# Optimization experiments

Measured on AMD Instinct MI355X. Metric: run time of the kernel, lower is better.

## Reference

```python
import jax, jax.numpy as jnp
import numpy as np
import math

NUM_EMBED = 1024
EMBED_DIM = 256
COMMITMENT_COST = 0.25


def setup_inputs() -> dict:
    key = jax.random.key(0)
    k1, k2 = jax.random.split(key)
    inputs = jax.random.normal(k1, (16, EMBED_DIM, 4096), dtype=jnp.float32)
    embed = jax.random.normal(k2, (NUM_EMBED, EMBED_DIM), dtype=jnp.float32)
    return {"inputs": inputs, "embed": embed}


def reference(inputs, embed):
    sg = jax.lax.stop_gradient
    num_embed = embed.shape[0]
    # channels-first (B, D, T) -> (B, T, D)
    x = jnp.swapaxes(inputs, 1, -1)
    B, T, D = x.shape
    flat = x.reshape(-1, D)  # (N, D)
    # pairwise squared distances to the codebook: (N, K)
    d2 = (jnp.sum(flat * flat, axis=1, keepdims=True)
          + jnp.sum(embed * embed, axis=1)
          - 2.0 * flat @ embed.T)
    q_idx = jnp.argmin(d2, axis=1)  # (N,) int
    # one-hot @ embed is just a gather of the nearest codewords
    z_q = embed[q_idx].reshape(x.shape)  # (B, T, D)
    vq_loss = jnp.mean((z_q - sg(x)) ** 2)
    commitment_loss = jnp.mean((sg(z_q) - x) ** 2)
    loss = vq_loss + COMMITMENT_COST * commitment_loss
    # straight-through estimator
    z_q_st = x + sg(z_q - x)
    # codebook usage stats: probs = mean of the one-hot rows
    n = flat.shape[0]
    probs = jnp.zeros((num_embed,), dtype=flat.dtype).at[q_idx].add(1.0) / n
    perplexity = jnp.exp(-jnp.sum(probs * jnp.log(probs + 1e-10)))
    num_spatial_positions = n / B  # == T
    kldiv_r = (math.log(num_embed) * num_spatial_positions
               * jnp.ones((B, 1), dtype=x.dtype))
    z_q_out = jnp.swapaxes(z_q_st, 1, -1)  # back to (B, D, T)
    return z_q_out, loss, kldiv_r, perplexity
```

## Files before the change

kernel.cpp:

```cpp
#include <hip/hip_runtime.h>
#include <math.h>

#define T_DIM 4096
#define D_DIM 256
#define K_NUM 1024
#define B_NUM 16
#define N_TOT (B_NUM * T_DIM)
#define EPS_FLAG 0.03f

typedef short short8 __attribute__((ext_vector_type(8)));
typedef float f32x4 __attribute__((ext_vector_type(4)));

#define WS_FLAGCNT 0
#define WS_LOSS 4
#define WS_HIST 64
#define WS_E2 4352
#define WS_QIDX 8704
#define WS_FLAGLIST 270848
#define WS_ESWZ 540672

__device__ inline unsigned short bf16r(float v) {
    unsigned u = __float_as_uint(v);
    unsigned r = u + 0x7FFFu + ((u >> 16) & 1u);
    return (unsigned short)(r >> 16);
}

__device__ inline void gl_lds16(const void* g, void* l) {
    __builtin_amdgcn_global_load_lds(
        (const __attribute__((address_space(1))) unsigned int*)g,
        (__attribute__((address_space(3))) unsigned int*)l, 16, 0, 0);
}

__global__ __launch_bounds__(256) void e2_kernel(const float* __restrict__ embed,
                                                 float* __restrict__ e2) {
    const int wave = threadIdx.x >> 6;
    const int lane = threadIdx.x & 63;
    const int k = blockIdx.x * 4 + wave;
    const float4* row = (const float4*)(embed + (size_t)k * D_DIM);
    float4 v = row[lane];
    float s = v.x * v.x + v.y * v.y + v.z * v.z + v.w * v.w;
    #pragma unroll
    for (int off = 32; off; off >>= 1) s += __shfl_down(s, off);
    if (lane == 0) e2[k] = s;
}

__global__ __launch_bounds__(256) void prep_eswz_kernel(const float* __restrict__ embed,
                                                        unsigned char* __restrict__ eswz) {
    const int tau = blockIdx.x * 256 + threadIdx.x;
    const int g = tau >> 9;
    const int k = (tau >> 6) & 7;
    const int l = tau & 63;
    const int col = g * 16 + (l & 15);
    const int d0 = k * 32 + ((l >> 4) << 3);
    const float* src = embed + (size_t)col * D_DIM + d0;
    short8 hi, lo;
    #pragma unroll
    for (int j = 0; j < 8; ++j) {
        float v = src[j];
        unsigned short hs = bf16r(v);
        float hif = __uint_as_float((unsigned)hs << 16);
        unsigned short ls = bf16r(v - hif);
        hi[j] = (short)hs; lo[j] = (short)ls;
    }
    *(short8*)(eswz + (size_t)g * 16384 + k * 1024 + l * 16) = hi;
    *(short8*)(eswz + (size_t)g * 16384 + 8192 + k * 1024 + l * 16) = lo;
}

__global__ __launch_bounds__(256, 2) void argmin_mfma_kernel(
    const float* __restrict__ x, const unsigned char* __restrict__ eswz,
    const float* __restrict__ e2, int* __restrict__ qidx,
    int* __restrict__ flagcnt, int* __restrict__ flaglist)
{
    __shared__ __align__(16) unsigned char bbuf[2][32768];
    __shared__ float e2s[K_NUM];

    const int tid = threadIdx.x;
    const int w = tid >> 6;
    const int l = tid & 63;
    const int rb = blockIdx.x * 128;
    const int b = rb >> 12;
    const float* xb = x + (size_t)b * (D_DIM * T_DIM);

    {
        const unsigned char* src = eswz + (size_t)tid * 16;
        #pragma unroll
        for (int r = 0; r < 8; ++r) gl_lds16(src + r * 4096, &bbuf[0][tid * 16 + r * 4096]);
    }
    for (int i = tid; i < K_NUM; i += 256) e2s[i] = e2[i];

    short8 Ah[2][8], Al[2][8];
    #pragma unroll
    for (int f = 0; f < 2; ++f) {
        const int row = rb + w * 32 + f * 16 + (l & 15);
        const int t = row & (T_DIM - 1);
        const float* xp = xb + t;
        #pragma unroll
        for (int k = 0; k < 8; ++k) {
            const int d0 = k * 32 + ((l >> 4) << 3);
            short8 hi, lo;
            #pragma unroll
            for (int j = 0; j < 8; ++j) {
                float v = xp[(size_t)(d0 + j) * T_DIM];
                unsigned short hs = bf16r(v);
                float hif = __uint_as_float((unsigned)hs << 16);
                unsigned short ls = bf16r(v - hif);
                hi[j] = (short)hs; lo[j] = (short)ls;
            }
            Ah[f][k] = hi; Al[f][k] = lo;
        }
    }
    __syncthreads();

    float bestv[8], secv[8];
    int   besti[8];
    #pragma unroll
    for (int s = 0; s < 8; ++s) { bestv[s] = 3.4e38f; secv[s] = 3.4e38f; besti[s] = 0x7FFFFFFF; }

    for (int g = 0; g < 32; ++g) {
        if (g + 1 < 32) {
            const unsigned char* src = eswz + (size_t)(g + 1) * 32768 + (size_t)tid * 16;
            unsigned char* dst = &bbuf[(g + 1) & 1][tid * 16];
            #pragma unroll
            for (int r = 0; r < 8; ++r) gl_lds16(src + r * 4096, dst + r * 4096);
        }
        const unsigned char* bb = bbuf[g & 1];

        f32x4 a00 = {0.f,0.f,0.f,0.f}, a01 = {0.f,0.f,0.f,0.f};
        f32x4 a10 = {0.f,0.f,0.f,0.f}, a11 = {0.f,0.f,0.f,0.f};
        #pragma unroll
        for (int k = 0; k < 8; ++k) {
            short8 bh0 = *(const short8*)(bb + k * 1024 + l * 16);
            short8 bl0 = *(const short8*)(bb + 8192 + k * 1024 + l * 16);
            short8 bh1 = *(const short8*)(bb + 16384 + k * 1024 + l * 16);
            short8 bl1 = *(const short8*)(bb + 16384 + 8192 + k * 1024 + l * 16);
            a00 = __builtin_amdgcn_mfma_f32_16x16x32_bf16(Ah[0][k], bh0, a00, 0, 0, 0);
            a10 = __builtin_amdgcn_mfma_f32_16x16x32_bf16(Ah[1][k], bh0, a10, 0, 0, 0);
            a01 = __builtin_amdgcn_mfma_f32_16x16x32_bf16(Ah[0][k], bh1, a01, 0, 0, 0);
            a11 = __builtin_amdgcn_mfma_f32_16x16x32_bf16(Ah[1][k], bh1, a11, 0, 0, 0);
            a00 = __builtin_amdgcn_mfma_f32_16x16x32_bf16(Al[0][k], bh0, a00, 0, 0, 0);
            a10 = __builtin_amdgcn_mfma_f32_16x16x32_bf16(Al[1][k], bh0, a10, 0, 0, 0);
            a01 = __builtin_amdgcn_mfma_f32_16x16x32_bf16(Al[0][k], bh1, a01, 0, 0, 0);
            a11 = __builtin_amdgcn_mfma_f32_16x16x32_bf16(Al[1][k], bh1, a11, 0, 0, 0);
            a00 = __builtin_amdgcn_mfma_f32_16x16x32_bf16(Ah[0][k], bl0, a00, 0, 0, 0);
            a10 = __builtin_amdgcn_mfma_f32_16x16x32_bf16(Ah[1][k], bl0, a10, 0, 0, 0);
            a01 = __builtin_amdgcn_mfma_f32_16x16x32_bf16(Ah[0][k], bl1, a01, 0, 0, 0);
            a11 = __builtin_amdgcn_mfma_f32_16x16x32_bf16(Ah[1][k], bl1, a11, 0, 0, 0);
        }

        const int col0 = g * 32 + (l & 15);
        const float e2a = e2s[col0];
        const float e2b = e2s[col0 + 16];
        #pragma unroll
        for (int f = 0; f < 2; ++f) {
            const f32x4 accA = f ? a10 : a00;
            const f32x4 accB = f ? a11 : a01;
            #pragma unroll
            for (int r = 0; r < 4; ++r) {
                const int s = f * 4 + r;
                float sA = fmaf(-2.f, accA[r], e2a);
                float sB = fmaf(-2.f, accB[r], e2b);
                bool swp = sB < sA;
                float lo = swp ? sB : sA;
                float hi = swp ? sA : sB;
                int   li = swp ? col0 + 16 : col0;
                bool upd = lo < bestv[s];
                float mx = upd ? bestv[s] : lo;
                bestv[s] = upd ? lo : bestv[s];
                besti[s] = upd ? li : besti[s];
                secv[s] = fminf(secv[s], fminf(mx, hi));
            }
        }
        __syncthreads();
    }

    #pragma unroll
    for (int slot = 0; slot < 8; ++slot) {
        float bv = bestv[slot], sv = secv[slot];
        int bi = besti[slot];
        #pragma unroll
        for (int d = 1; d < 16; d <<= 1) {
            float ob = __shfl_xor(bv, d);
            int   oi = __shfl_xor(bi, d);
            float os = __shfl_xor(sv, d);
            bool take = (ob < bv) || (ob == bv && oi < bi);
            float loser = take ? bv : ob;
            bv = take ? ob : bv;
            bi = take ? oi : bi;
            sv = fminf(fminf(sv, os), loser);
        }
        if ((l & 15) == 0) {
            const int row = rb + w * 32 + (slot >> 2) * 16 + (l >> 4) * 4 + (slot & 3);
            qidx[row] = bi;
            if (sv - bv < EPS_FLAG) {
                int p = atomicAdd(flagcnt, 1);
                flaglist[p] = row;
            }
        }
    }
}

__global__ __launch_bounds__(256) void cleanup_kernel(
    const float* __restrict__ x, const float* __restrict__ embed,
    const float* __restrict__ e2, const int* __restrict__ flagcnt,
    const int* __restrict__ flaglist, int* __restrict__ qidx)
{
    __shared__ float xr[256];
    __shared__ float rv[256];
    __shared__ int   rix[256];
    const int tid = threadIdx.x;
    int cnt = flagcnt[0];
    if (cnt > N_TOT) cnt = N_TOT;
    for (int it = blockIdx.x; it < cnt; it += gridDim.x) {
        const int row = flaglist[it];
        const int b = row >> 12, t = row & (T_DIM - 1);
        __syncthreads();
        xr[tid] = x[(size_t)b * (D_DIM * T_DIM) + (size_t)tid * T_DIM + t];
        __syncthreads();
        float best = 3.4e38f; int bi = 0x7FFFFFFF;
        for (int q = 0; q < 4; ++q) {
            const int c = q * 256 + tid;
            const float4* ep = (const float4*)(embed + (size_t)c * D_DIM);
            float acc = 0.f;
            #pragma unroll 8
            for (int dd = 0; dd < 64; ++dd) {
                float4 ev = ep[dd];
                acc = fmaf(ev.x, xr[dd * 4 + 0], acc);
                acc = fmaf(ev.y, xr[dd * 4 + 1], acc);
                acc = fmaf(ev.z, xr[dd * 4 + 2], acc);
                acc = fmaf(ev.w, xr[dd * 4 + 3], acc);
            }
            const float s = e2[c] - 2.f * acc;
            if (s < best || (s == best && c < bi)) { best = s; bi = c; }
        }
        rv[tid] = best; rix[tid] = bi;
        __syncthreads();
        for (int off = 128; off; off >>= 1) {
            if (tid < off) {
                float ov = rv[tid + off]; int oi = rix[tid + off];
                if (ov < rv[tid] || (ov == rv[tid] && oi < rix[tid])) { rv[tid] = ov; rix[tid] = oi; }
            }
            __syncthreads();
        }
        if (tid == 0) qidx[row] = rix[0];
    }
}

__global__ __launch_bounds__(256) void gather_kernel(
    const float* __restrict__ x, const float* __restrict__ embed,
    const int* __restrict__ qidx, float* __restrict__ out,
    float* __restrict__ loss_sum, int* __restrict__ hist)
{
    const int tid = threadIdx.x;
    const int n = blockIdx.x * 256 + tid;
    const int b = n >> 12, t = n & (T_DIM - 1);
    const int d0 = blockIdx.y * 64;
    const int idx = qidx[n];
    if (blockIdx.y == 0) atomicAdd(&hist[idx], 1);

    const float4* ep = (const float4*)(embed + (size_t)idx * D_DIM + d0);
    const float* xp = x + (size_t)b * (D_DIM * T_DIM) + (size_t)d0 * T_DIM + t;
    float*       op = out + (size_t)b * (D_DIM * T_DIM) + (size_t)d0 * T_DIM + t;

    float local = 0.f;
    #pragma unroll 4
    for (int i = 0; i < 16; ++i) {
        const float4 ev = ep[i];
        const size_t dd = (size_t)i * 4;
        float xv0 = xp[(dd + 0) * T_DIM];
        float xv1 = xp[(dd + 1) * T_DIM];
        float xv2 = xp[(dd + 2) * T_DIM];
        float xv3 = xp[(dd + 3) * T_DIM];
        op[(dd + 0) * T_DIM] = ev.x;
        op[(dd + 1) * T_DIM] = ev.y;
        op[(dd + 2) * T_DIM] = ev.z;
        op[(dd + 3) * T_DIM] = ev.w;
        float f0 = ev.x - xv0, f1 = ev.y - xv1, f2 = ev.z - xv2, f3 = ev.w - xv3;
        local = fmaf(f0, f0, local);
        local = fmaf(f1, f1, local);
        local = fmaf(f2, f2, local);
        local = fmaf(f3, f3, local);
    }
    #pragma unroll
    for (int off = 32; off; off >>= 1) local += __shfl_down(local, off);
    __shared__ float ls[4];
    if ((tid & 63) == 0) ls[tid >> 6] = local;
    __syncthreads();
    if (tid == 0) atomicAdd(loss_sum, ls[0] + ls[1] + ls[2] + ls[3]);
}

__global__ __launch_bounds__(256) void finalize_kernel(
    const int* __restrict__ hist, const float* __restrict__ loss_sum,
    float* __restrict__ out)
{
    const int tid = threadIdx.x;
    float acc = 0.f;
    #pragma unroll
    for (int i = tid; i < K_NUM; i += 256) {
        const float p = (float)hist[i] * (1.f / (float)N_TOT);
        acc += p * logf(p + 1e-10f);
    }
    #pragma unroll
    for (int off = 32; off; off >>= 1) acc += __shfl_down(acc, off);
    __shared__ float ls[4];
    if ((tid & 63) == 0) ls[tid >> 6] = acc;
    __syncthreads();
    if (tid == 0) {
        const float H = -(ls[0] + ls[1] + ls[2] + ls[3]);
        const size_t base = (size_t)N_TOT * D_DIM;
        out[base] = 1.25f * loss_sum[0] * (1.f / 16777216.f);
        const float kld = (float)(6.931471805599453 * 4096.0);
        #pragma unroll
        for (int i = 0; i < 16; ++i) out[base + 1 + i] = kld;
        out[base + 17] = expf(H);
    }
}

extern "C" void kernel_launch(void* const* d_in, const int* in_sizes, int n_in,
                              void* d_out, int out_size, void* d_ws, size_t ws_size,
                              hipStream_t stream)
{
    const float* x     = (const float*)d_in[0];
    const float* embed = (const float*)d_in[1];
    float* out = (float*)d_out;

    char* ws = (char*)d_ws;
    int*   flagcnt  = (int*)(ws + WS_FLAGCNT);
    float* loss_sum = (float*)(ws + WS_LOSS);
    int*   hist     = (int*)(ws + WS_HIST);
    float* e2       = (float*)(ws + WS_E2);
    int*   qidx     = (int*)(ws + WS_QIDX);
    int*   flaglist = (int*)(ws + WS_FLAGLIST);
    unsigned char* eswz = (unsigned char*)(ws + WS_ESWZ);

    hipMemsetAsync(ws, 0, 4160, stream);

    e2_kernel<<<K_NUM / 4, 256, 0, stream>>>(embed, e2);
    prep_eswz_kernel<<<128, 256, 0, stream>>>(embed, eswz);
    argmin_mfma_kernel<<<N_TOT / 128, 256, 0, stream>>>(x, eswz, e2, qidx, flagcnt, flaglist);
    cleanup_kernel<<<256, 256, 0, stream>>>(x, embed, e2, flagcnt, flaglist, qidx);
    gather_kernel<<<dim3(N_TOT / 256, 4), 256, 0, stream>>>(x, embed, qidx, out, loss_sum, hist);
    finalize_kernel<<<1, 256, 0, stream>>>(hist, loss_sum, out);
}
```

Baseline: 294.2 us.

## Switch argmin to single fp16 MFMA pass and fold loss into argmin

Replaces the three-pass bf16 hi/lo split GEMM with a single fp16 MFMA pass, which cuts MFMA work and LDS traffic by about a third to a half. The flag threshold is widened to compensate for the lower precision, so more rows go to the exact fp32 cleanup. Cleanup now batches 8 flagged rows per block so each embed row load is reused. The loss is computed from the argmin distance plus ||x||^2, with cleanup adding corrections, so the gather kernel no longer re-reads x. The risk is many more flagged rows and a less exact loss from the fp16 distance values.

```diff
diff --git a/kernel.cpp b/kernel.cpp
--- a/kernel.cpp
+++ b/kernel.cpp
@@ -6,10 +6,10 @@
 #define K_NUM 1024
 #define B_NUM 16
 #define N_TOT (B_NUM * T_DIM)
-#define EPS_FLAG 0.03f
-
-typedef short short8 __attribute__((ext_vector_type(8)));
+#define EPS_FLAG 0.35f
+
 typedef float f32x4 __attribute__((ext_vector_type(4)));
+typedef _Float16 half8 __attribute__((ext_vector_type(8)));
 
 #define WS_FLAGCNT 0
 #define WS_LOSS 4
@@ -17,13 +17,8 @@
 #define WS_E2 4352
 #define WS_QIDX 8704
 #define WS_FLAGLIST 270848
-#define WS_ESWZ 540672
-
-__device__ inline unsigned short bf16r(float v) {
-    unsigned u = __float_as_uint(v);
-    unsigned r = u + 0x7FFFu + ((u >> 16) & 1u);
-    return (unsigned short)(r >> 16);
-}
+#define WS_BESTD 532992
+#define WS_ESWZ 795136
 
 __device__ inline void gl_lds16(const void* g, void* l) {
     __builtin_amdgcn_global_load_lds(
@@ -53,25 +48,19 @@
     const int col = g * 16 + (l & 15);
     const int d0 = k * 32 + ((l >> 4) << 3);
     const float* src = embed + (size_t)col * D_DIM + d0;
-    short8 hi, lo;
-    #pragma unroll
-    for (int j = 0; j < 8; ++j) {
-        float v = src[j];
-        unsigned short hs = bf16r(v);
-        float hif = __uint_as_float((unsigned)hs << 16);
-        unsigned short ls = bf16r(v - hif);
-        hi[j] = (short)hs; lo[j] = (short)ls;
-    }
-    *(short8*)(eswz + (size_t)g * 16384 + k * 1024 + l * 16) = hi;
-    *(short8*)(eswz + (size_t)g * 16384 + 8192 + k * 1024 + l * 16) = lo;
+    half8 h;
+    #pragma unroll
+    for (int j = 0; j < 8; ++j) h[j] = (_Float16)src[j];
+    *(half8*)(eswz + (size_t)g * 8192 + k * 1024 + l * 16) = h;
 }
 
 __global__ __launch_bounds__(256, 2) void argmin_mfma_kernel(
     const float* __restrict__ x, const unsigned char* __restrict__ eswz,
     const float* __restrict__ e2, int* __restrict__ qidx,
-    int* __restrict__ flagcnt, int* __restrict__ flaglist)
-{
-    __shared__ __align__(16) unsigned char bbuf[2][32768];
+    int* __restrict__ flagcnt, int* __restrict__ flaglist,
+    float* __restrict__ bestd, float* __restrict__ loss_sum)
+{
+    __shared__ __align__(16) unsigned char bbuf[2][16384];
     __shared__ float e2s[K_NUM];
 
     const int tid = threadIdx.x;
@@ -84,30 +73,36 @@
     {
         const unsigned char* src = eswz + (size_t)tid * 16;
         #pragma unroll
-        for (int r = 0; r < 8; ++r) gl_lds16(src + r * 4096, &bbuf[0][tid * 16 + r * 4096]);
+        for (int r = 0; r < 4; ++r) gl_lds16(src + r * 4096, &bbuf[0][tid * 16 + r * 4096]);
     }
     for (int i = tid; i < K_NUM; i += 256) e2s[i] = e2[i];
 
-    short8 Ah[2][8], Al[2][8];
+    half8 Ah[2][8];
+    float x2v[2];
     #pragma unroll
     for (int f = 0; f < 2; ++f) {
         const int row = rb + w * 32 + f * 16 + (l & 15);
         const int t = row & (T_DIM - 1);
         const float* xp = xb + t;
+        float s2 = 0.f;
         #pragma unroll
         for (int k = 0; k < 8; ++k) {
             const int d0 = k * 32 + ((l >> 4) << 3);
-            short8 hi, lo;
+            half8 h;
             #pragma unroll
             for (int j = 0; j < 8; ++j) {
                 float v = xp[(size_t)(d0 + j) * T_DIM];
-                unsigned short hs = bf16r(v);
-                float hif = __uint_as_float((unsigned)hs << 16);
-                unsigned short ls = bf16r(v - hif);
-                hi[j] = (short)hs; lo[j] = (short)ls;
-            }
-            Ah[f][k] = hi; Al[f][k] = lo;
-        }
+                h[j] = (_Float16)v;
+                s2 = fmaf(v, v, s2);
+            }
+            Ah[f][k] = h;
+        }
+        x2v[f] = s2;
+    }
+    #pragma unroll
+    for (int f = 0; f < 2; ++f) {
+        x2v[f] += __shfl_xor(x2v[f], 16);
+        x2v[f] += __shfl_xor(x2v[f], 32);
     }
     __syncthreads();
 
@@ -118,10 +113,10 @@
 
     for (int g = 0; g < 32; ++g) {
         if (g + 1 < 32) {
-            const unsigned char* src = eswz + (size_t)(g + 1) * 32768 + (size_t)tid * 16;
+            const unsigned char* src = eswz + (size_t)(g + 1) * 16384 + (size_t)tid * 16;
             unsigned char* dst = &bbuf[(g + 1) & 1][tid * 16];
             #pragma unroll
-            for (int r = 0; r < 8; ++r) gl_lds16(src + r * 4096, dst + r * 4096);
+            for (int r = 0; r < 4; ++r) gl_lds16(src + r * 4096, dst + r * 4096);
         }
         const unsigned char* bb = bbuf[g & 1];
 
@@ -129,22 +124,12 @@
         f32x4 a10 = {0.f,0.f,0.f,0.f}, a11 = {0.f,0.f,0.f,0.f};
         #pragma unroll
         for (int k = 0; k < 8; ++k) {
-            short8 bh0 = *(const short8*)(bb + k * 1024 + l * 16);
-            short8 bl0 = *(const short8*)(bb + 8192 + k * 1024 + l * 16);
-            short8 bh1 = *(const short8*)(bb + 16384 + k * 1024 + l * 16);
-            short8 bl1 = *(const short8*)(bb + 16384 + 8192 + k * 1024 + l * 16);
-            a00 = __builtin_amdgcn_mfma_f32_16x16x32_bf16(Ah[0][k], bh0, a00, 0, 0, 0);
-            a10 = __builtin_amdgcn_mfma_f32_16x16x32_bf16(Ah[1][k], bh0, a10, 0, 0, 0);
-            a01 = __builtin_amdgcn_mfma_f32_16x16x32_bf16(Ah[0][k], bh1, a01, 0, 0, 0);
-            a11 = __builtin_amdgcn_mfma_f32_16x16x32_bf16(Ah[1][k], bh1, a11, 0, 0, 0);
-            a00 = __builtin_amdgcn_mfma_f32_16x16x32_bf16(Al[0][k], bh0, a00, 0, 0, 0);
-            a10 = __builtin_amdgcn_mfma_f32_16x16x32_bf16(Al[1][k], bh0, a10, 0, 0, 0);
-            a01 = __builtin_amdgcn_mfma_f32_16x16x32_bf16(Al[0][k], bh1, a01, 0, 0, 0);
-            a11 = __builtin_amdgcn_mfma_f32_16x16x32_bf16(Al[1][k], bh1, a11, 0, 0, 0);
-            a00 = __builtin_amdgcn_mfma_f32_16x16x32_bf16(Ah[0][k], bl0, a00, 0, 0, 0);
-            a10 = __builtin_amdgcn_mfma_f32_16x16x32_bf16(Ah[1][k], bl0, a10, 0, 0, 0);
-            a01 = __builtin_amdgcn_mfma_f32_16x16x32_bf16(Ah[0][k], bl1, a01, 0, 0, 0);
-            a11 = __builtin_amdgcn_mfma_f32_16x16x32_bf16(Ah[1][k], bl1, a11, 0, 0, 0);
+            half8 b0 = *(const half8*)(bb + k * 1024 + l * 16);
+            half8 b1 = *(const half8*)(bb + 8192 + k * 1024 + l * 16);
+            a00 = __builtin_amdgcn_mfma_f32_16x16x32_f16(Ah[0][k], b0, a00, 0, 0, 0);
+            a10 = __builtin_amdgcn_mfma_f32_16x16x32_f16(Ah[1][k], b0, a10, 0, 0, 0);
+            a01 = __builtin_amdgcn_mfma_f32_16x16x32_f16(Ah[0][k], b1, a01, 0, 0, 0);
+            a11 = __builtin_amdgcn_mfma_f32_16x16x32_f16(Ah[1][k], b1, a11, 0, 0, 0);
         }
 
         const int col0 = g * 32 + (l & 15);
@@ -173,6 +158,7 @@
         __syncthreads();
     }
 
+    float lossw = 0.f;
     #pragma unroll
     for (int slot = 0; slot < 8; ++slot) {
         float bv = bestv[slot], sv = secv[slot];
@@ -188,67 +174,111 @@
             bi = take ? oi : bi;
             sv = fminf(fminf(sv, os), loser);
         }
+        const int srcl = ((l >> 4) << 2) + (slot & 3);
+        const float x2r = __shfl(x2v[slot >> 2], srcl);
         if ((l & 15) == 0) {
             const int row = rb + w * 32 + (slot >> 2) * 16 + (l >> 4) * 4 + (slot & 3);
             qidx[row] = bi;
+            lossw += bv + x2r;
             if (sv - bv < EPS_FLAG) {
+                bestd[row] = bv;
                 int p = atomicAdd(flagcnt, 1);
                 flaglist[p] = row;
             }
         }
     }
+    lossw += __shfl_down(lossw, 16);
+    lossw += __shfl_down(lossw, 32);
+    if (l == 0) atomicAdd(loss_sum, lossw);
 }
 
 __global__ __launch_bounds__(256) void cleanup_kernel(
     const float* __restrict__ x, const float* __restrict__ embed,
     const float* __restrict__ e2, const int* __restrict__ flagcnt,
-    const int* __restrict__ flaglist, int* __restrict__ qidx)
-{
-    __shared__ float xr[256];
-    __shared__ float rv[256];
-    __shared__ int   rix[256];
+    const int* __restrict__ flaglist, int* __restrict__ qidx,
+    const float* __restrict__ bestd, float* __restrict__ loss_sum)
+{
+    __shared__ float xr[8][256];
+    __shared__ float rvall[8][256];
+    __shared__ int   rixall[8][256];
     const int tid = threadIdx.x;
     int cnt = flagcnt[0];
     if (cnt > N_TOT) cnt = N_TOT;
-    for (int it = blockIdx.x; it < cnt; it += gridDim.x) {
-        const int row = flaglist[it];
-        const int b = row >> 12, t = row & (T_DIM - 1);
+    for (int base = blockIdx.x * 8; base < cnt; base += gridDim.x * 8) {
+        const int nr = (cnt - base < 8) ? (cnt - base) : 8;
         __syncthreads();
-        xr[tid] = x[(size_t)b * (D_DIM * T_DIM) + (size_t)tid * T_DIM + t];
+        #pragma unroll
+        for (int r = 0; r < 8; ++r) {
+            float v = 0.f;
+            if (r < nr) {
+                const int row = flaglist[base + r];
+                const int bb = row >> 12, t = row & (T_DIM - 1);
+                v = x[(size_t)bb * (D_DIM * T_DIM) + (size_t)tid * T_DIM + t];
+            }
+            xr[r][tid] = v;
+        }
         __syncthreads();
-        float best = 3.4e38f; int bi = 0x7FFFFFFF;
+
+        float bv[8]; int bix[8];
+        #pragma unroll
+        for (int r = 0; r < 8; ++r) { bv[r] = 3.4e38f; bix[r] = 0x7FFFFFFF; }
         for (int q = 0; q < 4; ++q) {
             const int c = q * 256 + tid;
             const float4* ep = (const float4*)(embed + (size_t)c * D_DIM);
-            float acc = 0.f;
-            #pragma unroll 8
+            float acc[8];
+            #pragma unroll
+            for (int r = 0; r < 8; ++r) acc[r] = 0.f;
+            #pragma unroll 4
             for (int dd = 0; dd < 64; ++dd) {
-                float4 ev = ep[dd];
-                acc = fmaf(ev.x, xr[dd * 4 + 0], acc);
-                acc = fmaf(ev.y, xr[dd * 4 + 1], acc);
-                acc = fmaf(ev.z, xr[dd * 4 + 2], acc);
-                acc = fmaf(ev.w, xr[dd * 4 + 3], acc);
-            }
-            const float s = e2[c] - 2.f * acc;
-            if (s < best || (s == best && c < bi)) { best = s; bi = c; }
-        }
-        rv[tid] = best; rix[tid] = bi;
+                const float4 ev = ep[dd];
+                #pragma unroll
+                for (int r = 0; r < 8; ++r) {
+                    const float4 xv = *(const float4*)&xr[r][dd * 4];
+                    acc[r] = fmaf(ev.x, xv.x, acc[r]);
+                    acc[r] = fmaf(ev.y, xv.y, acc[r]);
+                    acc[r] = fmaf(ev.z, xv.z, acc[r]);
+                    acc[r] = fmaf(ev.w, xv.w, acc[r]);
+                }
+            }
+            const float ec = e2[c];
+            #pragma unroll
+            for (int r = 0; r < 8; ++r) {
+                const float s = fmaf(-2.f, acc[r], ec);
+                if (s < bv[r] || (s == bv[r] && c < bix[r])) { bv[r] = s; bix[r] = c; }
+            }
+        }
+        #pragma unroll
+        for (int r = 0; r < 8; ++r) { rvall[r][tid] = bv[r]; rixall[r][tid] = bix[r]; }
         __syncthreads();
-        for (int off = 128; off; off >>= 1) {
-            if (tid < off) {
-                float ov = rv[tid + off]; int oi = rix[tid + off];
-                if (ov < rv[tid] || (ov == rv[tid] && oi < rix[tid])) { rv[tid] = ov; rix[tid] = oi; }
-            }
-            __syncthreads();
-        }
-        if (tid == 0) qidx[row] = rix[0];
+        const int w = tid >> 6, ll = tid & 63;
+        #pragma unroll
+        for (int rr = 0; rr < 2; ++rr) {
+            const int r = w * 2 + rr;
+            float mv = 3.4e38f; int mi = 0x7FFFFFFF;
+            #pragma unroll
+            for (int j = 0; j < 4; ++j) {
+                const float v = rvall[r][ll + j * 64];
+                const int i2 = rixall[r][ll + j * 64];
+                if (v < mv || (v == mv && i2 < mi)) { mv = v; mi = i2; }
+            }
+            #pragma unroll
+            for (int d = 1; d < 64; d <<= 1) {
+                const float ov = __shfl_xor(mv, d);
+                const int   oi = __shfl_xor(mi, d);
+                if (ov < mv || (ov == mv && oi < mi)) { mv = ov; mi = oi; }
+            }
+            if (ll == 0 && r < nr) {
+                const int row = flaglist[base + r];
+                qidx[row] = mi;
+                atomicAdd(loss_sum, mv - bestd[row]);
+            }
+        }
     }
 }
 
 __global__ __launch_bounds__(256) void gather_kernel(
-    const float* __restrict__ x, const float* __restrict__ embed,
-    const int* __restrict__ qidx, float* __restrict__ out,
-    float* __restrict__ loss_sum, int* __restrict__ hist)
+    const float* __restrict__ embed, const int* __restrict__ qidx,
+    float* __restrict__ out, int* __restrict__ hist)
 {
     const int tid = threadIdx.x;
     const int n = blockIdx.x * 256 + tid;
@@ -258,34 +288,16 @@
     if (blockIdx.y == 0) atomicAdd(&hist[idx], 1);
 
     const float4* ep = (const float4*)(embed + (size_t)idx * D_DIM + d0);
-    const float* xp = x + (size_t)b * (D_DIM * T_DIM) + (size_t)d0 * T_DIM + t;
-    float*       op = out + (size_t)b * (D_DIM * T_DIM) + (size_t)d0 * T_DIM + t;
-
-    float local = 0.f;
+    float*        op = out + (size_t)b * (D_DIM * T_DIM) + (size_t)d0 * T_DIM + t;
     #pragma unroll 4
     for (int i = 0; i < 16; ++i) {
         const float4 ev = ep[i];
         const size_t dd = (size_t)i * 4;
-        float xv0 = xp[(dd + 0) * T_DIM];
-        float xv1 = xp[(dd + 1) * T_DIM];
-        float xv2 = xp[(dd + 2) * T_DIM];
-        float xv3 = xp[(dd + 3) * T_DIM];
         op[(dd + 0) * T_DIM] = ev.x;
         op[(dd + 1) * T_DIM] = ev.y;
         op[(dd + 2) * T_DIM] = ev.z;
         op[(dd + 3) * T_DIM] = ev.w;
-        float f0 = ev.x - xv0, f1 = ev.y - xv1, f2 = ev.z - xv2, f3 = ev.w - xv3;
-        local = fmaf(f0, f0, local);
-        local = fmaf(f1, f1, local);
-        local = fmaf(f2, f2, local);
-        local = fmaf(f3, f3, local);
-    }
-    #pragma unroll
-    for (int off = 32; off; off >>= 1) local += __shfl_down(local, off);
-    __shared__ float ls[4];
-    if ((tid & 63) == 0) ls[tid >> 6] = local;
-    __syncthreads();
-    if (tid == 0) atomicAdd(loss_sum, ls[0] + ls[1] + ls[2] + ls[3]);
+    }
 }
 
 __global__ __launch_bounds__(256) void finalize_kernel(
@@ -330,14 +342,17 @@
     float* e2       = (float*)(ws + WS_E2);
     int*   qidx     = (int*)(ws + WS_QIDX);
     int*   flaglist = (int*)(ws + WS_FLAGLIST);
+    float* bestd    = (float*)(ws + WS_BESTD);
     unsigned char* eswz = (unsigned char*)(ws + WS_ESWZ);
 
     hipMemsetAsync(ws, 0, 4160, stream);
 
     e2_kernel<<<K_NUM / 4, 256, 0, stream>>>(embed, e2);
     prep_eswz_kernel<<<128, 256, 0, stream>>>(embed, eswz);
-    argmin_mfma_kernel<<<N_TOT / 128, 256, 0, stream>>>(x, eswz, e2, qidx, flagcnt, flaglist);
-    cleanup_kernel<<<256, 256, 0, stream>>>(x, embed, e2, flagcnt, flaglist, qidx);
-    gather_kernel<<<dim3(N_TOT / 256, 4), 256, 0, stream>>>(x, embed, qidx, out, loss_sum, hist);
+    argmin_mfma_kernel<<<N_TOT / 128, 256, 0, stream>>>(x, eswz, e2, qidx, flagcnt, flaglist,
+                                                        bestd, loss_sum);
+    cleanup_kernel<<<256, 256, 0, stream>>>(x, embed, e2, flagcnt, flaglist, qidx,
+                                            bestd, loss_sum);
+    gather_kernel<<<dim3(N_TOT / 256, 4), 256, 0, stream>>>(embed, qidx, out, hist);
     finalize_kernel<<<1, 256, 0, stream>>>(hist, loss_sum, out);
 }
```

Measured after the change: 403.4 us. 1.37x slower.
